# Optimization experiments

Hardware: AMD Instinct MI355X
Metric: run time of the kernel (lower is better)

## Reference

```python
import jax, jax.numpy as jnp
import numpy as np

N_HEADS = 16
HEAD_DIM = 64
STRIDE = 32  # default local_attention_ctx used as stride in 'strided' mode


def _strided_fill_mask(n):
    # Faithful to the torch code: positions where (i >= j) and ((i - j) % stride == 0)
    # get mask value 1, and the code does masked_fill_(mask == 1, -inf),
    # i.e. those positions are set to -inf (inverted polarity, replicated as-is).
    i = jnp.arange(n)[:, None]
    j = jnp.arange(n)[None, :]
    return (i >= j) & (((i - j) % STRIDE) == 0)  # [n, n] bool, True -> -inf


def setup_inputs() -> dict:
    key = jax.random.key(0)
    k_x, k_qkv, k_out = jax.random.split(key, 3)
    b, n, c = 2, 2048, 1024
    inner = N_HEADS * HEAD_DIM  # 1024
    x = jax.random.normal(k_x, (b, n, c), dtype=jnp.float32)
    W_qkv = jax.random.normal(k_qkv, (c, 3 * inner), dtype=jnp.float32) * 0.02
    W_out = jax.random.normal(k_out, (inner, c), dtype=jnp.float32) * 0.02
    b_out = jnp.zeros((c,), dtype=jnp.float32)
    return {"x": x, "W_qkv": W_qkv, "W_out": W_out, "b_out": b_out}


def reference(x, W_qkv, W_out, b_out):
    b, n, c = x.shape
    h, hd = N_HEADS, HEAD_DIM
    scale = c ** (-0.5)  # n_embeddings ** -0.5, as in the original

    qkv = x @ W_qkv                              # [b, n, 3*h*hd]
    q, k, v = jnp.split(qkv, 3, axis=-1)
    def to_heads(t):
        return t.reshape(b, n, h, hd).transpose(0, 2, 1, 3)  # [b, h, n, hd]
    q, k, v = to_heads(q), to_heads(k), to_heads(v)

    dots = jnp.einsum('bhid,bhjd->bhij', q, k) * scale       # [b, h, n, n]
    fill = _strided_fill_mask(n)                             # [n, n]
    dots = jnp.where(fill[None, None], -jnp.inf, dots)

    attn = jax.nn.softmax(dots, axis=-1)
    out = jnp.einsum('bhij,bhjd->bhid', attn, v)             # [b, h, n, hd]
    out = out.transpose(0, 2, 1, 3).reshape(b, n, h * hd)    # [b, n, inner]
    out = out @ W_out + b_out                                # dropout: eval/identity
    return out
```

## Files before the change

kernel.cpp:

```cpp
#include <hip/hip_runtime.h>

typedef __attribute__((ext_vector_type(8))) short bf16x8;
typedef __attribute__((ext_vector_type(4))) float f32x4;

#if __has_builtin(__builtin_amdgcn_exp2f)
#define EXP2F(x) __builtin_amdgcn_exp2f(x)
#else
extern "C" __device__ float __ocml_native_exp2_f32(float);
#define EXP2F(x) __ocml_native_exp2_f32(x)
#endif

#define QSCALE 0.04508422002778011f
#define NS 2048

__device__ __forceinline__ ushort f32_to_bf16(float f) {
  union { float f; unsigned u; } x; x.f = f;
  unsigned r = x.u + 0x7fffu + ((x.u >> 16) & 1u);
  return (ushort)(r >> 16);
}

__device__ __forceinline__ unsigned pack_bf16(float f0, float f1) {
  union { float f; unsigned u; } a, b;
  a.f = f0; b.f = f1;
  return __builtin_amdgcn_perm(b.u + 0x8000u, a.u + 0x8000u, 0x07060302u);
}

__device__ __forceinline__ void load16_to_lds(const void* g, void* l) {
  __builtin_amdgcn_global_load_lds(
      (const __attribute__((address_space(1))) unsigned int*)(
          reinterpret_cast<uintptr_t>(g)),
      (__attribute__((address_space(3))) unsigned int*)(
          reinterpret_cast<uintptr_t>(l)),
      16, 0, 0);
}

__global__ __launch_bounds__(256) void prep(
    const float* __restrict__ x, const float* __restrict__ Wqkv,
    const float* __restrict__ Wout,
    ushort* __restrict__ xb, ushort* __restrict__ wqkvT,
    ushort* __restrict__ woutT)
{
  __shared__ ushort tile[32][33];
  const int bid = blockIdx.x, t = threadIdx.x;
  if (bid < 2048) {
    size_t i = (size_t)bid * 256 + t;
    const float4* p = (const float4*)(x + i * 8);
    float4 a = p[0], b = p[1];
    union { uint4 v; ushort s[8]; } u;
    u.s[0] = f32_to_bf16(a.x); u.s[1] = f32_to_bf16(a.y);
    u.s[2] = f32_to_bf16(a.z); u.s[3] = f32_to_bf16(a.w);
    u.s[4] = f32_to_bf16(b.x); u.s[5] = f32_to_bf16(b.y);
    u.s[6] = f32_to_bf16(b.z); u.s[7] = f32_to_bf16(b.w);
    *(uint4*)(xb + i * 8) = u.v;
  } else if (bid < 5120) {
    int tb = bid - 2048;
    int cb = (tb % 96) * 32, rb = (tb / 96) * 32;
    int tx = t & 31, ty = t >> 5;
    float s = (cb + tx) < 1024 ? QSCALE : 1.0f;
#pragma unroll
    for (int k = 0; k < 4; ++k)
      tile[ty + 8 * k][tx] =
          f32_to_bf16(Wqkv[(size_t)(rb + ty + 8 * k) * 3072 + cb + tx] * s);
    __syncthreads();
#pragma unroll
    for (int k = 0; k < 4; ++k)
      wqkvT[(size_t)(cb + ty + 8 * k) * 1024 + rb + tx] = tile[tx][ty + 8 * k];
  } else {
    int tb = bid - 5120;
    int cb = (tb & 31) * 32, rb = (tb >> 5) * 32;
    int tx = t & 31, ty = t >> 5;
#pragma unroll
    for (int k = 0; k < 4; ++k)
      tile[ty + 8 * k][tx] =
          f32_to_bf16(Wout[(size_t)(rb + ty + 8 * k) * 1024 + cb + tx]);
    __syncthreads();
#pragma unroll
    for (int k = 0; k < 4; ++k)
      woutT[(size_t)(cb + ty + 8 * k) * 1024 + rb + tx] = tile[tx][ty + 8 * k];
  }
}

template <int TM, int BK>
__device__ __forceinline__ void stage_ab(
    const ushort* __restrict__ A, const ushort* __restrict__ Bt,
    int K, int mbase, int nbase, int kb,
    ushort* __restrict__ sA, ushort* __restrict__ sB,
    int w, int lrow, int gofs)
{
  constexpr int ROWS = (BK == 32) ? 16 : 8;
#pragma unroll
  for (int r = 0; r < TM / (ROWS * 4); ++r) {
    int rb = w * (TM / 4) + r * ROWS;
    load16_to_lds(&A[(size_t)(mbase + rb + lrow) * K + kb + gofs], &sA[rb * BK]);
  }
#pragma unroll
  for (int r = 0; r < 128 / (ROWS * 4); ++r) {
    int rb = w * 32 + r * ROWS;
    load16_to_lds(&Bt[(size_t)(nbase + rb + lrow) * K + kb + gofs], &sB[rb * BK]);
  }
}

template <int TM, int BK, typename TC>
__device__ __forceinline__ void gemm_core(
    const ushort* __restrict__ A, const ushort* __restrict__ Bt,
    const float* __restrict__ bias, TC* __restrict__ C,
    int N, int K, int mbase, int nbase,
    ushort* __restrict__ sA0, ushort* __restrict__ sB0,
    ushort* __restrict__ sA1, ushort* __restrict__ sB1)
{
  constexpr int MT = TM / 32;
  const int t = threadIdx.x;
  const int lane = t & 63, w = t >> 6;
  const int quad = lane >> 4, l16 = lane & 15;
  const int wr = w >> 1, wc = w & 1;
  const int lrow = (BK == 32) ? (lane >> 2) : (lane >> 3);
  const int gofs = (BK == 32)
      ? (((lane & 3) ^ ((lane >> 3) & 3)) * 8)
      : (((lane & 7) ^ (lane >> 3)) * 8);
  const int rswz = (BK == 32) ? ((l16 >> 1) & 3) : (l16 & 7);

  f32x4 acc[MT][4];
#pragma unroll
  for (int i = 0; i < MT; ++i)
#pragma unroll
    for (int j = 0; j < 4; ++j)
      acc[i][j] = (f32x4){0.f, 0.f, 0.f, 0.f};

  stage_ab<TM, BK>(A, Bt, K, mbase, nbase, 0, sA0, sB0, w, lrow, gofs);

  for (int kb = 0; kb < K; kb += BK) {
    const bool odd = (kb / BK) & 1;
    ushort* sA = odd ? sA1 : sA0;
    ushort* sB = odd ? sB1 : sB0;
    ushort* pA = odd ? sA0 : sA1;
    ushort* pB = odd ? sB0 : sB1;
    __syncthreads();
    if (kb + BK < K)
      stage_ab<TM, BK>(A, Bt, K, mbase, nbase, kb + BK, pA, pB, w, lrow, gofs);

#pragma unroll
    for (int c = 0; c < BK / 32; ++c) {
      bf16x8 af[MT], bfr[4];
#pragma unroll
      for (int mt = 0; mt < MT; ++mt)
        af[mt] = *(const bf16x8*)&sA[(wr * (TM / 2) + mt * 16 + l16) * BK +
                                     (((c * 4 + quad) ^ rswz) * 8)];
#pragma unroll
      for (int nt = 0; nt < 4; ++nt)
        bfr[nt] = *(const bf16x8*)&sB[(wc * 64 + nt * 16 + l16) * BK +
                                      (((c * 4 + quad) ^ rswz) * 8)];
#pragma unroll
      for (int mt = 0; mt < MT; ++mt)
#pragma unroll
        for (int nt = 0; nt < 4; ++nt)
          acc[mt][nt] = __builtin_amdgcn_mfma_f32_16x16x32_bf16(
              af[mt], bfr[nt], acc[mt][nt], 0, 0, 0);
    }
  }

#pragma unroll
  for (int mt = 0; mt < MT; ++mt) {
#pragma unroll
    for (int nt = 0; nt < 4; ++nt) {
      int col = nbase + wc * 64 + nt * 16 + l16;
      float bv = bias ? bias[col] : 0.f;
#pragma unroll
      for (int ri = 0; ri < 4; ++ri) {
        int row = mbase + wr * (TM / 2) + mt * 16 + quad * 4 + ri;
        float val = acc[mt][nt][ri] + bv;
        if constexpr (__is_same(TC, float))
          C[(size_t)row * N + col] = val;
        else
          C[(size_t)row * N + col] = f32_to_bf16(val);
      }
    }
  }
}

__global__ __launch_bounds__(256) void gemm_qkvt(
    const ushort* __restrict__ xb, const ushort* __restrict__ wqkvT,
    ushort* __restrict__ qk, ushort* __restrict__ vtbuf)
{
  __shared__ ushort sA0[128 * 32], sB0[128 * 32];
  __shared__ ushort sA1[128 * 32], sB1[128 * 32];
  const int bid = blockIdx.x;
  if (bid < 512) {
    gemm_core<128, 32, ushort>(xb, wqkvT, nullptr, qk, 2048, 1024,
                               (bid >> 4) * 128, (bid & 15) * 128,
                               sA0, sB0, sA1, sB1);
  } else {
    const int id = bid - 512;
    gemm_core<128, 32, ushort>(wqkvT + (size_t)2048 * 1024, xb, nullptr, vtbuf,
                               4096, 1024, (id >> 5) * 128, (id & 31) * 128,
                               sA0, sB0, sA1, sB1);
  }
}

__global__ __launch_bounds__(256) void gemm_out(
    const ushort* __restrict__ attnb, const ushort* __restrict__ woutT,
    const float* __restrict__ bias, float* __restrict__ out)
{
  __shared__ ushort sA0[64 * 64], sB0[128 * 64];
  __shared__ ushort sA1[64 * 64], sB1[128 * 64];
  const int bid = blockIdx.x;
  gemm_core<64, 64, float>(attnb, woutT, bias, out, 1024, 1024,
                           (bid >> 3) * 64, (bid & 7) * 128,
                           sA0, sB0, sA1, sB1);
}

__device__ __forceinline__ void stage_kv(
    const ushort* __restrict__ qk, const ushort* __restrict__ vt,
    ushort* sKb, ushort* sVb, int b, int h, int kvbase,
    int w, int rowK, int csw)
{
#pragma unroll
  for (int g = 0; g < 2; ++g) {
    int rk = w * 16 + g * 8 + rowK;
    load16_to_lds(&qk[((size_t)(b * NS + kvbase + rk)) * 2048 + 1024 + h * 64 + csw],
                  &sKb[(w * 16 + g * 8) * 64]);
    load16_to_lds(&vt[((size_t)(h * 64 + rk)) * 4096 + b * 2048 + kvbase + csw],
                  &sVb[(w * 16 + g * 8) * 64]);
  }
}

__global__ __launch_bounds__(256) void attn_kernel(
    const ushort* __restrict__ qk, const ushort* __restrict__ vt,
    ushort* __restrict__ attn_out)
{
  __shared__ ushort sK[2][64 * 64];
  __shared__ ushort sV[2][64 * 64];
  __shared__ ushort sPt[4][32][72];

  const int t = threadIdx.x;
  const int lane = t & 63, w = t >> 6;
  const int quad = lane >> 4, l16 = lane & 15;
  const int bh = blockIdx.y, b = bh >> 4, h = bh & 15;
  const int qbase = blockIdx.x * 128;
  const int rowK = lane >> 3;
  const int csw = ((lane & 7) ^ rowK) * 8;
  const int swz = l16 & 7;

  bf16x8 qf[2][2];
#pragma unroll
  for (int is = 0; is < 2; ++is)
#pragma unroll
    for (int c = 0; c < 2; ++c)
      qf[is][c] = *(const bf16x8*)&qk[
          ((size_t)(b * NS + qbase + w * 32 + is * 16 + l16)) * 2048 +
          h * 64 + c * 32 + quad * 8];

  bf16x8 ones;
  { union { bf16x8 v; ushort s[8]; } ou;
#pragma unroll
    for (int i = 0; i < 8; ++i) ou.s[i] = 0x3F80;
    ones = ou.v; }

  unsigned amask[2][4][2];
#pragma unroll
  for (int is = 0; is < 2; ++is)
#pragma unroll
    for (int mt = 0; mt < 4; ++mt)
#pragma unroll
      for (int hf = 0; hf < 2; ++hf) {
        int r0 = hf * 2, r1 = hf * 2 + 1;
        int base = is * 16 + l16 - mt * 16 - quad * 4;
        unsigned m = 0xFFFFFFFFu;
        if (((base - r0) & 31) == 0) m &= 0xFFFF0000u;
        if (((base - r1) & 31) == 0) m &= 0x0000FFFFu;
        amask[is][mt][hf] = m;
      }

  const int ib64 = (qbase + w * 32) >> 6;

  f32x4 oacc[2][4];
#pragma unroll
  for (int is = 0; is < 2; ++is)
#pragma unroll
    for (int dt = 0; dt < 4; ++dt) oacc[is][dt] = (f32x4){0.f, 0.f, 0.f, 0.f};
  f32x4 lsum[2];
  lsum[0] = (f32x4){0.f, 0.f, 0.f, 0.f};
  lsum[1] = (f32x4){0.f, 0.f, 0.f, 0.f};

  stage_kv(qk, vt, sK[0], sV[0], b, h, 0, w, rowK, csw);

  for (int kb = 0; kb < NS / 64; ++kb) {
    const int cur = kb & 1;
    const int kvbase = kb * 64;
    __syncthreads();
    if (kb < NS / 64 - 1)
      stage_kv(qk, vt, sK[cur ^ 1], sV[cur ^ 1], b, h, kvbase + 64, w, rowK, csw);

    const ushort* K = sK[cur];
    const ushort* V = sV[cur];

    f32x4 st[2][4];
#pragma unroll
    for (int is = 0; is < 2; ++is)
#pragma unroll
      for (int mt = 0; mt < 4; ++mt) st[is][mt] = (f32x4){0.f, 0.f, 0.f, 0.f};
#pragma unroll
    for (int mt = 0; mt < 4; ++mt)
#pragma unroll
      for (int c = 0; c < 2; ++c) {
        bf16x8 kf = *(const bf16x8*)&K[(mt * 16 + l16) * 64 +
                                       (((c * 4 + quad) ^ swz) * 8)];
        st[0][mt] = __builtin_amdgcn_mfma_f32_16x16x32_bf16(
            kf, qf[0][c], st[0][mt], 0, 0, 0);
        st[1][mt] = __builtin_amdgcn_mfma_f32_16x16x32_bf16(
            kf, qf[1][c], st[1][mt], 0, 0, 0);
      }

    if (kb < ib64) {
#pragma unroll
      for (int is = 0; is < 2; ++is)
#pragma unroll
        for (int mt = 0; mt < 4; ++mt) {
          unsigned lo = pack_bf16(EXP2F(st[is][mt][0]), EXP2F(st[is][mt][1])) &
                        amask[is][mt][0];
          unsigned hi = pack_bf16(EXP2F(st[is][mt][2]), EXP2F(st[is][mt][3])) &
                        amask[is][mt][1];
          *(uint2*)&sPt[w][is * 16 + l16][mt * 16 + quad * 4] =
              make_uint2(lo, hi);
        }
    } else if (kb > ib64) {
#pragma unroll
      for (int is = 0; is < 2; ++is)
#pragma unroll
        for (int mt = 0; mt < 4; ++mt) {
          unsigned lo = pack_bf16(EXP2F(st[is][mt][0]), EXP2F(st[is][mt][1]));
          unsigned hi = pack_bf16(EXP2F(st[is][mt][2]), EXP2F(st[is][mt][3]));
          *(uint2*)&sPt[w][is * 16 + l16][mt * 16 + quad * 4] =
              make_uint2(lo, hi);
        }
    } else {
#pragma unroll
      for (int is = 0; is < 2; ++is) {
        int irow = qbase + w * 32 + is * 16 + l16;
#pragma unroll
        for (int mt = 0; mt < 4; ++mt) {
          float p[4];
#pragma unroll
          for (int ri = 0; ri < 4; ++ri) {
            int j = kvbase + mt * 16 + quad * 4 + ri;
            p[ri] = EXP2F(st[is][mt][ri]);
            unsigned du = (unsigned)(irow - j);
            if ((du & 0x8000001Fu) == 0u) p[ri] = 0.f;
          }
          unsigned lo = pack_bf16(p[0], p[1]);
          unsigned hi = pack_bf16(p[2], p[3]);
          *(uint2*)&sPt[w][is * 16 + l16][mt * 16 + quad * 4] =
              make_uint2(lo, hi);
        }
      }
    }

#pragma unroll
    for (int c2 = 0; c2 < 2; ++c2) {
      bf16x8 vf[4];
#pragma unroll
      for (int dt = 0; dt < 4; ++dt)
        vf[dt] = *(const bf16x8*)&V[(dt * 16 + l16) * 64 +
                                    (((c2 * 4 + quad) ^ swz) * 8)];
#pragma unroll
      for (int is = 0; is < 2; ++is) {
        bf16x8 pf = *(const bf16x8*)&sPt[w][is * 16 + l16][c2 * 32 + quad * 8];
        lsum[is] = __builtin_amdgcn_mfma_f32_16x16x32_bf16(
            pf, ones, lsum[is], 0, 0, 0);
#pragma unroll
        for (int dt = 0; dt < 4; ++dt)
          oacc[is][dt] = __builtin_amdgcn_mfma_f32_16x16x32_bf16(
              pf, vf[dt], oacc[is][dt], 0, 0, 0);
      }
    }
  }

#pragma unroll
  for (int is = 0; is < 2; ++is)
#pragma unroll
    for (int ri = 0; ri < 4; ++ri) {
      float inv = __builtin_amdgcn_rcpf(lsum[is][ri]);
      int ig = qbase + w * 32 + is * 16 + quad * 4 + ri;
#pragma unroll
      for (int dt = 0; dt < 4; ++dt)
        attn_out[(size_t)(b * NS + ig) * 1024 + h * 64 + dt * 16 + l16] =
            f32_to_bf16(oacc[is][dt][ri] * inv);
    }
}

extern "C" void kernel_launch(void* const* d_in, const int* in_sizes, int n_in,
                              void* d_out, int out_size, void* d_ws, size_t ws_size,
                              hipStream_t stream) {
  const float* x    = (const float*)d_in[0];
  const float* Wqkv = (const float*)d_in[1];
  const float* Wout = (const float*)d_in[2];
  const float* bout = (const float*)d_in[3];
  float* out = (float*)d_out;

  ushort* qk    = (ushort*)d_ws;
  ushort* vt    = qk + (size_t)4096 * 2048;
  ushort* xb    = vt + (size_t)1024 * 4096;
  ushort* wqkvT = xb + (size_t)4096 * 1024;
  ushort* woutT = wqkvT + (size_t)3072 * 1024;
  ushort* attnb = xb;

  prep<<<6144, 256, 0, stream>>>(x, Wqkv, Wout, xb, wqkvT, woutT);
  gemm_qkvt<<<768, 256, 0, stream>>>(xb, wqkvT, qk, vt);
  attn_kernel<<<dim3(NS / 128, 32), 256, 0, stream>>>(qk, vt, attnb);
  gemm_out<<<512, 256, 0, stream>>>(attnb, woutT, bout, out);
}
```

Before: 188.3 us.

## Split attention across 8 waves of 16 rows and reorder GEMM block mapping

The attention kernel now launches 512 threads per block, so each of 8 waves handles 16 query rows instead of 32. Each thread's register footprint shrinks and the K/V staging is spread over more waves, which should raise occupancy and latency hiding. The cost is that K/V fragments are reloaded from LDS once per 16 rows instead of once per 32. Separately, the two GEMM kernels remap block indices so that neighbouring blocks share A/B tiles for better L2 reuse, and gemm_qkvt gets a launch-bounds occupancy hint.

```diff
diff --git a/kernel.cpp b/kernel.cpp
--- a/kernel.cpp
+++ b/kernel.cpp
@@ -177,7 +177,7 @@
   }
 }
 
-__global__ __launch_bounds__(256) void gemm_qkvt(
+__global__ __launch_bounds__(256, 3) void gemm_qkvt(
     const ushort* __restrict__ xb, const ushort* __restrict__ wqkvT,
     ushort* __restrict__ qk, ushort* __restrict__ vtbuf)
 {
@@ -185,13 +185,15 @@
   __shared__ ushort sA1[128 * 32], sB1[128 * 32];
   const int bid = blockIdx.x;
   if (bid < 512) {
+    int j = bid >> 3;
+    int m = (bid & 7) * 4 + (j & 3);
+    int n = j >> 2;
     gemm_core<128, 32, ushort>(xb, wqkvT, nullptr, qk, 2048, 1024,
-                               (bid >> 4) * 128, (bid & 15) * 128,
-                               sA0, sB0, sA1, sB1);
+                               m * 128, n * 128, sA0, sB0, sA1, sB1);
   } else {
     const int id = bid - 512;
     gemm_core<128, 32, ushort>(wqkvT + (size_t)2048 * 1024, xb, nullptr, vtbuf,
-                               4096, 1024, (id >> 5) * 128, (id & 31) * 128,
+                               4096, 1024, (id & 7) * 128, (id >> 3) * 128,
                                sA0, sB0, sA1, sB1);
   }
 }
@@ -203,9 +205,10 @@
   __shared__ ushort sA0[64 * 64], sB0[128 * 64];
   __shared__ ushort sA1[64 * 64], sB1[128 * 64];
   const int bid = blockIdx.x;
+  int m = (bid & 7) * 8 + ((bid >> 3) & 7);
+  int n = bid >> 6;
   gemm_core<64, 64, float>(attnb, woutT, bias, out, 1024, 1024,
-                           (bid >> 3) * 64, (bid & 7) * 128,
-                           sA0, sB0, sA1, sB1);
+                           m * 64, n * 128, sA0, sB0, sA1, sB1);
 }
 
 __device__ __forceinline__ void stage_kv(
@@ -213,23 +216,20 @@
     ushort* sKb, ushort* sVb, int b, int h, int kvbase,
     int w, int rowK, int csw)
 {
-#pragma unroll
-  for (int g = 0; g < 2; ++g) {
-    int rk = w * 16 + g * 8 + rowK;
-    load16_to_lds(&qk[((size_t)(b * NS + kvbase + rk)) * 2048 + 1024 + h * 64 + csw],
-                  &sKb[(w * 16 + g * 8) * 64]);
-    load16_to_lds(&vt[((size_t)(h * 64 + rk)) * 4096 + b * 2048 + kvbase + csw],
-                  &sVb[(w * 16 + g * 8) * 64]);
-  }
-}
-
-__global__ __launch_bounds__(256) void attn_kernel(
+  int rk = w * 8 + rowK;
+  load16_to_lds(&qk[((size_t)(b * NS + kvbase + rk)) * 2048 + 1024 + h * 64 + csw],
+                &sKb[(w * 8) * 64]);
+  load16_to_lds(&vt[((size_t)(h * 64 + rk)) * 4096 + b * 2048 + kvbase + csw],
+                &sVb[(w * 8) * 64]);
+}
+
+__global__ __launch_bounds__(512, 4) void attn_kernel(
     const ushort* __restrict__ qk, const ushort* __restrict__ vt,
     ushort* __restrict__ attn_out)
 {
   __shared__ ushort sK[2][64 * 64];
   __shared__ ushort sV[2][64 * 64];
-  __shared__ ushort sPt[4][32][72];
+  __shared__ ushort sPt[8][16][72];
 
   const int t = threadIdx.x;
   const int lane = t & 63, w = t >> 6;
@@ -240,14 +240,12 @@
   const int csw = ((lane & 7) ^ rowK) * 8;
   const int swz = l16 & 7;
 
-  bf16x8 qf[2][2];
-#pragma unroll
-  for (int is = 0; is < 2; ++is)
-#pragma unroll
-    for (int c = 0; c < 2; ++c)
-      qf[is][c] = *(const bf16x8*)&qk[
-          ((size_t)(b * NS + qbase + w * 32 + is * 16 + l16)) * 2048 +
-          h * 64 + c * 32 + quad * 8];
+  bf16x8 qf[2];
+#pragma unroll
+  for (int c = 0; c < 2; ++c)
+    qf[c] = *(const bf16x8*)&qk[
+        ((size_t)(b * NS + qbase + w * 16 + l16)) * 2048 +
+        h * 64 + c * 32 + quad * 8];
 
   bf16x8 ones;
   { union { bf16x8 v; ushort s[8]; } ou;
@@ -255,31 +253,25 @@
     for (int i = 0; i < 8; ++i) ou.s[i] = 0x3F80;
     ones = ou.v; }
 
-  unsigned amask[2][4][2];
-#pragma unroll
-  for (int is = 0; is < 2; ++is)
-#pragma unroll
-    for (int mt = 0; mt < 4; ++mt)
-#pragma unroll
-      for (int hf = 0; hf < 2; ++hf) {
-        int r0 = hf * 2, r1 = hf * 2 + 1;
-        int base = is * 16 + l16 - mt * 16 - quad * 4;
-        unsigned m = 0xFFFFFFFFu;
-        if (((base - r0) & 31) == 0) m &= 0xFFFF0000u;
-        if (((base - r1) & 31) == 0) m &= 0x0000FFFFu;
-        amask[is][mt][hf] = m;
-      }
-
-  const int ib64 = (qbase + w * 32) >> 6;
-
-  f32x4 oacc[2][4];
-#pragma unroll
-  for (int is = 0; is < 2; ++is)
-#pragma unroll
-    for (int dt = 0; dt < 4; ++dt) oacc[is][dt] = (f32x4){0.f, 0.f, 0.f, 0.f};
-  f32x4 lsum[2];
-  lsum[0] = (f32x4){0.f, 0.f, 0.f, 0.f};
-  lsum[1] = (f32x4){0.f, 0.f, 0.f, 0.f};
+  unsigned amask[4][2];
+#pragma unroll
+  for (int mt = 0; mt < 4; ++mt)
+#pragma unroll
+    for (int hf = 0; hf < 2; ++hf) {
+      int r0 = hf * 2, r1 = hf * 2 + 1;
+      int base = (w & 1) * 16 + l16 - mt * 16 - quad * 4;
+      unsigned m = 0xFFFFFFFFu;
+      if (((base - r0) & 31) == 0) m &= 0xFFFF0000u;
+      if (((base - r1) & 31) == 0) m &= 0x0000FFFFu;
+      amask[mt][hf] = m;
+    }
+
+  const int ib64 = (qbase + w * 16) >> 6;
+
+  f32x4 oacc[4];
+#pragma unroll
+  for (int dt = 0; dt < 4; ++dt) oacc[dt] = (f32x4){0.f, 0.f, 0.f, 0.f};
+  f32x4 lsum = (f32x4){0.f, 0.f, 0.f, 0.f};
 
   stage_kv(qk, vt, sK[0], sV[0], b, h, 0, w, rowK, csw);
 
@@ -293,98 +285,76 @@
     const ushort* K = sK[cur];
     const ushort* V = sV[cur];
 
-    f32x4 st[2][4];
-#pragma unroll
-    for (int is = 0; is < 2; ++is)
-#pragma unroll
-      for (int mt = 0; mt < 4; ++mt) st[is][mt] = (f32x4){0.f, 0.f, 0.f, 0.f};
+    f32x4 st[4];
+#pragma unroll
+    for (int mt = 0; mt < 4; ++mt) st[mt] = (f32x4){0.f, 0.f, 0.f, 0.f};
 #pragma unroll
     for (int mt = 0; mt < 4; ++mt)
 #pragma unroll
       for (int c = 0; c < 2; ++c) {
         bf16x8 kf = *(const bf16x8*)&K[(mt * 16 + l16) * 64 +
                                        (((c * 4 + quad) ^ swz) * 8)];
-        st[0][mt] = __builtin_amdgcn_mfma_f32_16x16x32_bf16(
-            kf, qf[0][c], st[0][mt], 0, 0, 0);
-        st[1][mt] = __builtin_amdgcn_mfma_f32_16x16x32_bf16(
-            kf, qf[1][c], st[1][mt], 0, 0, 0);
+        st[mt] = __builtin_amdgcn_mfma_f32_16x16x32_bf16(
+            kf, qf[c], st[mt], 0, 0, 0);
       }
 
     if (kb < ib64) {
 #pragma unroll
-      for (int is = 0; is < 2; ++is)
-#pragma unroll
-        for (int mt = 0; mt < 4; ++mt) {
-          unsigned lo = pack_bf16(EXP2F(st[is][mt][0]), EXP2F(st[is][mt][1])) &
-                        amask[is][mt][0];
-          unsigned hi = pack_bf16(EXP2F(st[is][mt][2]), EXP2F(st[is][mt][3])) &
-                        amask[is][mt][1];
-          *(uint2*)&sPt[w][is * 16 + l16][mt * 16 + quad * 4] =
-              make_uint2(lo, hi);
+      for (int mt = 0; mt < 4; ++mt) {
+        unsigned lo = pack_bf16(EXP2F(st[mt][0]), EXP2F(st[mt][1])) &
+                      amask[mt][0];
+        unsigned hi = pack_bf16(EXP2F(st[mt][2]), EXP2F(st[mt][3])) &
+                      amask[mt][1];
+        *(uint2*)&sPt[w][l16][mt * 16 + quad * 4] = make_uint2(lo, hi);
+      }
+    } else if (kb > ib64) {
+#pragma unroll
+      for (int mt = 0; mt < 4; ++mt) {
+        unsigned lo = pack_bf16(EXP2F(st[mt][0]), EXP2F(st[mt][1]));
+        unsigned hi = pack_bf16(EXP2F(st[mt][2]), EXP2F(st[mt][3]));
+        *(uint2*)&sPt[w][l16][mt * 16 + quad * 4] = make_uint2(lo, hi);
+      }
+    } else {
+      int irow = qbase + w * 16 + l16;
+#pragma unroll
+      for (int mt = 0; mt < 4; ++mt) {
+        float p[4];
+#pragma unroll
+        for (int ri = 0; ri < 4; ++ri) {
+          int j = kvbase + mt * 16 + quad * 4 + ri;
+          p[ri] = EXP2F(st[mt][ri]);
+          unsigned du = (unsigned)(irow - j);
+          if ((du & 0x8000001Fu) == 0u) p[ri] = 0.f;
         }
-    } else if (kb > ib64) {
-#pragma unroll
-      for (int is = 0; is < 2; ++is)
-#pragma unroll
-        for (int mt = 0; mt < 4; ++mt) {
-          unsigned lo = pack_bf16(EXP2F(st[is][mt][0]), EXP2F(st[is][mt][1]));
-          unsigned hi = pack_bf16(EXP2F(st[is][mt][2]), EXP2F(st[is][mt][3]));
-          *(uint2*)&sPt[w][is * 16 + l16][mt * 16 + quad * 4] =
-              make_uint2(lo, hi);
-        }
-    } else {
-#pragma unroll
-      for (int is = 0; is < 2; ++is) {
-        int irow = qbase + w * 32 + is * 16 + l16;
-#pragma unroll
-        for (int mt = 0; mt < 4; ++mt) {
-          float p[4];
-#pragma unroll
-          for (int ri = 0; ri < 4; ++ri) {
-            int j = kvbase + mt * 16 + quad * 4 + ri;
-            p[ri] = EXP2F(st[is][mt][ri]);
-            unsigned du = (unsigned)(irow - j);
-            if ((du & 0x8000001Fu) == 0u) p[ri] = 0.f;
-          }
-          unsigned lo = pack_bf16(p[0], p[1]);
-          unsigned hi = pack_bf16(p[2], p[3]);
-          *(uint2*)&sPt[w][is * 16 + l16][mt * 16 + quad * 4] =
-              make_uint2(lo, hi);
-        }
+        unsigned lo = pack_bf16(p[0], p[1]);
+        unsigned hi = pack_bf16(p[2], p[3]);
+        *(uint2*)&sPt[w][l16][mt * 16 + quad * 4] = make_uint2(lo, hi);
       }
     }
 
 #pragma unroll
     for (int c2 = 0; c2 < 2; ++c2) {
-      bf16x8 vf[4];
-#pragma unroll
-      for (int dt = 0; dt < 4; ++dt)
-        vf[dt] = *(const bf16x8*)&V[(dt * 16 + l16) * 64 +
-                                    (((c2 * 4 + quad) ^ swz) * 8)];
-#pragma unroll
-      for (int is = 0; is < 2; ++is) {
-        bf16x8 pf = *(const bf16x8*)&sPt[w][is * 16 + l16][c2 * 32 + quad * 8];
-        lsum[is] = __builtin_amdgcn_mfma_f32_16x16x32_bf16(
-            pf, ones, lsum[is], 0, 0, 0);
-#pragma unroll
-        for (int dt = 0; dt < 4; ++dt)
-          oacc[is][dt] = __builtin_amdgcn_mfma_f32_16x16x32_bf16(
-              pf, vf[dt], oacc[is][dt], 0, 0, 0);
-      }
-    }
-  }
-
-#pragma unroll
-  for (int is = 0; is < 2; ++is)
-#pragma unroll
-    for (int ri = 0; ri < 4; ++ri) {
-      float inv = __builtin_amdgcn_rcpf(lsum[is][ri]);
-      int ig = qbase + w * 32 + is * 16 + quad * 4 + ri;
-#pragma unroll
-      for (int dt = 0; dt < 4; ++dt)
-        attn_out[(size_t)(b * NS + ig) * 1024 + h * 64 + dt * 16 + l16] =
-            f32_to_bf16(oacc[is][dt][ri] * inv);
-    }
+      bf16x8 pf = *(const bf16x8*)&sPt[w][l16][c2 * 32 + quad * 8];
+      lsum = __builtin_amdgcn_mfma_f32_16x16x32_bf16(pf, ones, lsum, 0, 0, 0);
+#pragma unroll
+      for (int dt = 0; dt < 4; ++dt) {
+        bf16x8 vf = *(const bf16x8*)&V[(dt * 16 + l16) * 64 +
+                                       (((c2 * 4 + quad) ^ swz) * 8)];
+        oacc[dt] = __builtin_amdgcn_mfma_f32_16x16x32_bf16(
+            pf, vf, oacc[dt], 0, 0, 0);
+      }
+    }
+  }
+
+#pragma unroll
+  for (int ri = 0; ri < 4; ++ri) {
+    float inv = __builtin_amdgcn_rcpf(lsum[ri]);
+    int ig = qbase + w * 16 + quad * 4 + ri;
+#pragma unroll
+    for (int dt = 0; dt < 4; ++dt)
+      attn_out[(size_t)(b * NS + ig) * 1024 + h * 64 + dt * 16 + l16] =
+          f32_to_bf16(oacc[dt][ri] * inv);
+  }
 }
 
 extern "C" void kernel_launch(void* const* d_in, const int* in_sizes, int n_in,
@@ -405,6 +375,6 @@
 
   prep<<<6144, 256, 0, stream>>>(x, Wqkv, Wout, xb, wqkvT, woutT);
   gemm_qkvt<<<768, 256, 0, stream>>>(xb, wqkvT, qk, vt);
-  attn_kernel<<<dim3(NS / 128, 32), 256, 0, stream>>>(qk, vt, attnb);
+  attn_kernel<<<dim3(NS / 128, 32), 512, 0, stream>>>(qk, vt, attnb);
   gemm_out<<<512, 256, 0, stream>>>(attnb, woutT, bout, out);
 }
```

Measured after the change: 174.6 us. 1.08x faster.
